# Kernel optimization log

Hardware: AMD Instinct MI355X
Metric: run time of the kernel (lower is better)

Reference implementation:

```python
import jax, jax.numpy as jnp
import numpy as np

B, S, H, E, K = 8, 4096, 1024, 256, 64
NEG = -1e30  # finite stand-in for -inf to keep grads NaN-free


def setup_inputs() -> dict:
    key = jax.random.key(0)
    ks = jax.random.split(key, 8)
    Hq = H // 4
    sc = 0.02
    return {
        "hidden_states": jax.random.normal(ks[0], (B, S, H), dtype=jnp.float32),
        "attention_mask": jnp.ones((B, S), dtype=jnp.int32),
        "block_boundaries": jnp.sort(jax.random.randint(ks[1], (B, K), 0, S), axis=-1),
        "tok_w1": jax.random.normal(ks[2], (H, Hq), dtype=jnp.float32) * sc,
        "tok_b1": jnp.zeros((Hq,), dtype=jnp.float32),
        "tok_w2": jax.random.normal(ks[3], (Hq, 1), dtype=jnp.float32) * sc,
        "tok_b2": jnp.zeros((1,), dtype=jnp.float32),
        "blk_w1": jax.random.normal(ks[4], (H, Hq), dtype=jnp.float32) * sc,
        "blk_b1": jnp.zeros((Hq,), dtype=jnp.float32),
        "blk_w2": jax.random.normal(ks[5], (Hq, 1), dtype=jnp.float32) * sc,
        "blk_b2": jnp.zeros((1,), dtype=jnp.float32),
        "out_w": jax.random.normal(ks[6], (H, E), dtype=jnp.float32) * sc,
        "out_b": jnp.zeros((E,), dtype=jnp.float32),
    }


def _attn_scores(x, w1, b1, w2, b2):
    # Linear -> Tanh -> Linear(.,1), squeeze last dim
    return (jnp.tanh(x @ w1 + b1) @ w2 + b2)[..., 0]


def reference(hidden_states, attention_mask, block_boundaries,
              tok_w1, tok_b1, tok_w2, tok_b2,
              blk_w1, blk_b1, blk_w2, blk_b2,
              out_w, out_b):
    Bz, Sz, Hz = hidden_states.shape
    Kz = block_boundaries.shape[1]
    pos = jnp.arange(Sz)
    # token -> block id: last boundary <= pos (tokens before first boundary get -1)
    block_id = jax.vmap(lambda bnd: jnp.searchsorted(bnd, pos, side='right') - 1)(block_boundaries)  # [B,S]
    member = block_id[:, :, None] == jnp.arange(Kz)[None, None, :]      # [B,S,K]
    valid = (attention_mask == 1) & (block_id >= 0)                     # [B,S]
    m_full = member & valid[:, :, None]                                 # [B,S,K]

    # stage 1: per-block masked softmax over tokens
    tok_scores = _attn_scores(hidden_states, tok_w1, tok_b1, tok_w2, tok_b2)  # [B,S]
    s = jnp.where(m_full, tok_scores[:, :, None], NEG)
    mx = jnp.max(s, axis=1, keepdims=True)                              # [B,1,K]
    e = jnp.where(m_full, jnp.exp(tok_scores[:, :, None] - mx), 0.0)
    denom = jnp.sum(e, axis=1, keepdims=True)                           # [B,1,K]
    w = jnp.where(denom > 0, e / jnp.maximum(denom, 1e-30), 0.0)
    block_embed = jnp.einsum('bsk,bsd->bkd', w, hidden_states)          # [B,K,H]
    block_valid = denom[:, 0, :] > 0                                    # [B,K] (empty blocks dropped)

    # stage 2: softmax over (non-empty) blocks
    blk_scores = _attn_scores(block_embed, blk_w1, blk_b1, blk_w2, blk_b2)    # [B,K]
    blk_scores = jnp.where(block_valid, blk_scores, NEG)
    bw = jax.nn.softmax(blk_scores, axis=-1)
    func = jnp.einsum('bk,bkd->bd', bw, block_embed)                    # [B,H]

    out = func @ out_w + out_b                                          # [B,E]
    return out / jnp.maximum(jnp.linalg.norm(out, axis=-1, keepdims=True), 1e-12)
```

## Files before the change

kernel.cpp:

```cpp
#include <hip/hip_runtime.h>
#include <math.h>

#define BB 8
#define SS 4096
#define HH 1024
#define EE 256
#define KK 64
#define HQ 256
#define NEGF -1e30f

typedef short bf16x8 __attribute__((ext_vector_type(8)));
typedef float f32x4  __attribute__((ext_vector_type(4)));

__device__ inline short f2bf(float x) {
    unsigned u = __float_as_uint(x);
    unsigned r = (u + 0x7fffu + ((u >> 16) & 1u)) >> 16;
    return (short)r;
}

__device__ inline unsigned pk2bf(float lo, float hi) {
    unsigned a = __float_as_uint(lo) + 0x8000u;
    unsigned b = __float_as_uint(hi) + 0x8000u;
    return (a >> 16) | (b & 0xffff0000u);
}

__global__ __launch_bounds__(256) void convert_w1_kernel(
    const float* __restrict__ w1, short* __restrict__ w1s)
{
    const int kb = blockIdx.x, n = threadIdx.x;
    for (int kk = 0; kk < 32; kk++)
        w1s[kb * 8192 + n * 32 + kk] = f2bf(w1[(kb * 32 + kk) * HQ + n]);
}

__global__ __launch_bounds__(256) void mfma_score3_kernel(
    const float* __restrict__ X, const short* __restrict__ w1s,
    const float* __restrict__ b1, const float* __restrict__ w2,
    const float* __restrict__ b2, float* __restrict__ out)
{
    __shared__ __attribute__((aligned(16))) short As[2][2048];
    __shared__ float part[4][64];

    const int t = threadIdx.x;
    const int wv = t >> 6, lane = t & 63, lo = lane & 15, q = lane >> 4;
    const long row0 = (long)blockIdx.x * 64;

    f32x4 acc[4][4];
#pragma unroll
    for (int i = 0; i < 4; i++)
#pragma unroll
        for (int j = 0; j < 4; j++) acc[i][j] = (f32x4){0.f, 0.f, 0.f, 0.f};

    const float* xs = X + (row0 + wv * 16 + lo) * HH + q * 8;
    const short* wp = w1s + (wv * 64 + lo) * 32 + q * 8;

    {
        const float4* p = (const float4*)xs;
        float4 v0 = p[0], v1 = p[1];
        union { unsigned u[4]; bf16x8 h; } c;
        c.u[0] = pk2bf(v0.x, v0.y); c.u[1] = pk2bf(v0.z, v0.w);
        c.u[2] = pk2bf(v1.x, v1.y); c.u[3] = pk2bf(v1.z, v1.w);
        *(bf16x8*)(&As[0][t * 8]) = c.h;
    }
    bf16x8 bA[4], bB[4];
#pragma unroll
    for (int ct = 0; ct < 4; ct++)
        bA[ct] = *(const bf16x8*)(wp + ct * 512);
    __syncthreads();

    for (int kb = 0; kb < 32; kb += 2) {
        {
            const int k1 = kb + 1;
            const float4* p = (const float4*)(xs + k1 * 32);
            float4 v0 = p[0], v1 = p[1];
#pragma unroll
            for (int ct = 0; ct < 4; ct++)
                bB[ct] = *(const bf16x8*)(wp + k1 * 8192 + ct * 512);
            bf16x8 af[4];
#pragma unroll
            for (int rt = 0; rt < 4; rt++)
                af[rt] = *(bf16x8*)(&As[0][(rt * 64 + q * 16 + lo) * 8]);
#pragma unroll
            for (int rt = 0; rt < 4; rt++)
#pragma unroll
                for (int ct = 0; ct < 4; ct++)
                    acc[rt][ct] = __builtin_amdgcn_mfma_f32_16x16x32_bf16(
                        af[rt], bA[ct], acc[rt][ct], 0, 0, 0);
            union { unsigned u[4]; bf16x8 h; } c;
            c.u[0] = pk2bf(v0.x, v0.y); c.u[1] = pk2bf(v0.z, v0.w);
            c.u[2] = pk2bf(v1.x, v1.y); c.u[3] = pk2bf(v1.z, v1.w);
            *(bf16x8*)(&As[1][t * 8]) = c.h;
        }
        __syncthreads();
        {
            const int k2 = (kb + 2 < 32) ? kb + 2 : 31;
            const float4* p = (const float4*)(xs + k2 * 32);
            float4 v0 = p[0], v1 = p[1];
#pragma unroll
            for (int ct = 0; ct < 4; ct++)
                bA[ct] = *(const bf16x8*)(wp + k2 * 8192 + ct * 512);
            bf16x8 af[4];
#pragma unroll
            for (int rt = 0; rt < 4; rt++)
                af[rt] = *(bf16x8*)(&As[1][(rt * 64 + q * 16 + lo) * 8]);
#pragma unroll
            for (int rt = 0; rt < 4; rt++)
#pragma unroll
                for (int ct = 0; ct < 4; ct++)
                    acc[rt][ct] = __builtin_amdgcn_mfma_f32_16x16x32_bf16(
                        af[rt], bB[ct], acc[rt][ct], 0, 0, 0);
            union { unsigned u[4]; bf16x8 h; } c;
            c.u[0] = pk2bf(v0.x, v0.y); c.u[1] = pk2bf(v0.z, v0.w);
            c.u[2] = pk2bf(v1.x, v1.y); c.u[3] = pk2bf(v1.z, v1.w);
            *(bf16x8*)(&As[0][t * 8]) = c.h;
        }
        __syncthreads();
    }

    float rowpart[4][4];
#pragma unroll
    for (int rt = 0; rt < 4; rt++)
#pragma unroll
        for (int r = 0; r < 4; r++) rowpart[rt][r] = 0.f;
#pragma unroll
    for (int ct = 0; ct < 4; ct++) {
        const int c = wv * 64 + ct * 16 + lo;
        const float b1c = b1[c], w2c = w2[c];
#pragma unroll
        for (int rt = 0; rt < 4; rt++)
#pragma unroll
            for (int r = 0; r < 4; r++)
                rowpart[rt][r] += tanhf(acc[rt][ct][r] + b1c) * w2c;
    }
#pragma unroll
    for (int rt = 0; rt < 4; rt++)
#pragma unroll
        for (int r = 0; r < 4; r++) {
            float v = rowpart[rt][r];
            v += __shfl_down(v, 8, 64);
            v += __shfl_down(v, 4, 64);
            v += __shfl_down(v, 2, 64);
            v += __shfl_down(v, 1, 64);
            rowpart[rt][r] = v;
        }
    if (lo == 0)
#pragma unroll
        for (int rt = 0; rt < 4; rt++)
#pragma unroll
            for (int r = 0; r < 4; r++)
                part[wv][rt * 16 + q * 4 + r] = rowpart[rt][r];
    __syncthreads();
    if (t < 64)
        out[row0 + t] = part[0][t] + part[1][t] + part[2][t] + part[3][t] + b2[0];
}

__global__ __launch_bounds__(256) void block_stats_kernel(
    const float* __restrict__ scores, const int* __restrict__ mask,
    const int* __restrict__ bnd, float* __restrict__ bmax, float* __restrict__ bden,
    float* __restrict__ wtok)
{
    const int b = blockIdx.x >> 6, k = blockIdx.x & 63;
    const int start = bnd[b * KK + k];
    const int end = (k == KK - 1) ? SS : bnd[b * KK + k + 1];
    const int tid = threadIdx.x;
    __shared__ float r[4];
    __shared__ float mshared, dshared;

    float m = NEGF;
    for (int s = start + tid; s < end; s += 256)
        if (mask[b * SS + s] == 1) m = fmaxf(m, scores[b * SS + s]);
    for (int off = 32; off > 0; off >>= 1) m = fmaxf(m, __shfl_down(m, off, 64));
    if ((tid & 63) == 0) r[tid >> 6] = m;
    __syncthreads();
    if (tid == 0) mshared = fmaxf(fmaxf(r[0], r[1]), fmaxf(r[2], r[3]));
    __syncthreads();
    m = mshared;

    float d = 0.f;
    for (int s = start + tid; s < end; s += 256)
        if (mask[b * SS + s] == 1) d += expf(scores[b * SS + s] - m);
    for (int off = 32; off > 0; off >>= 1) d += __shfl_down(d, off, 64);
    __syncthreads();
    if ((tid & 63) == 0) r[tid >> 6] = d;
    __syncthreads();
    if (tid == 0) {
        float den = r[0] + r[1] + r[2] + r[3];
        bmax[blockIdx.x] = m; bden[blockIdx.x] = den;
        dshared = (den > 0.f) ? 1.f / fmaxf(den, 1e-30f) : 0.f;
    }
    __syncthreads();
    const float inv = dshared;
    for (int s = start + tid; s < end; s += 256)
        wtok[b * SS + s] = (mask[b * SS + s] == 1) ? expf(scores[b * SS + s] - m) * inv : 0.f;
}

#define TCH 32
__global__ __launch_bounds__(256) void block_embed2_kernel(
    const float* __restrict__ hidden, const float* __restrict__ wtok,
    const int* __restrict__ bnd, float* __restrict__ embed)
{
    const int b = blockIdx.x >> 7;
    const int ch = blockIdx.x & 127;
    const int t = threadIdx.x;
    __shared__ int bsh[KK];
    if (t < KK) bsh[t] = bnd[b * KK + t];
    __syncthreads();

    const int s0 = ch * TCH, s1 = s0 + TCH;
    int cur = -1;
    for (int i = 0; i < KK; i++) if (bsh[i] <= s0) cur = i;

    float a0 = 0.f, a1 = 0.f, a2 = 0.f, a3 = 0.f;
    bool any = false;
    for (int s = s0; s < s1; s++) {
        while (cur + 1 < KK && bsh[cur + 1] <= s) {
            if (any) {
                float* e = embed + ((long)b * KK + cur) * HH;
                atomicAdd(e + t, a0); atomicAdd(e + t + 256, a1);
                atomicAdd(e + t + 512, a2); atomicAdd(e + t + 768, a3);
                a0 = a1 = a2 = a3 = 0.f; any = false;
            }
            cur++;
        }
        if (cur < 0) continue;
        const float w = wtok[b * SS + s];
        if (w != 0.f) {
            const float* hr = hidden + ((long)b * SS + s) * HH;
            a0 = fmaf(w, hr[t], a0);
            a1 = fmaf(w, hr[t + 256], a1);
            a2 = fmaf(w, hr[t + 512], a2);
            a3 = fmaf(w, hr[t + 768], a3);
            any = true;
        }
    }
    if (any) {
        float* e = embed + ((long)b * KK + cur) * HH;
        atomicAdd(e + t, a0); atomicAdd(e + t + 256, a1);
        atomicAdd(e + t + 512, a2); atomicAdd(e + t + 768, a3);
    }
}

__global__ __launch_bounds__(256) void finalize_a_kernel(
    const float* __restrict__ embed, const float* __restrict__ bscores,
    const float* __restrict__ bden, float* __restrict__ func)
{
    const int b = blockIdx.x, t = threadIdx.x;
    __shared__ float bw[KK];
    if (t < KK) {
        float s = (bden[b * KK + t] > 0.f) ? bscores[b * KK + t] : NEGF;
        float m = s;
        for (int off = 32; off > 0; off >>= 1) m = fmaxf(m, __shfl_xor(m, off, 64));
        float e = expf(s - m);
        float d = e;
        for (int off = 32; off > 0; off >>= 1) d += __shfl_xor(d, off, 64);
        bw[t] = e / d;
    }
    __syncthreads();
    float4 f = {0.f, 0.f, 0.f, 0.f};
    const float4* ep = (const float4*)(embed + (long)b * KK * HH) + t;
#pragma unroll 8
    for (int k = 0; k < KK; k++) {
        const float w = bw[k];
        const float4 h = ep[k * (HH / 4)];
        f.x = fmaf(w, h.x, f.x); f.y = fmaf(w, h.y, f.y);
        f.z = fmaf(w, h.z, f.z); f.w = fmaf(w, h.w, f.w);
    }
    *((float4*)(func + b * HH) + t) = f;
}

__global__ __launch_bounds__(256) void finalize_b_kernel(
    const float* __restrict__ func, const float* __restrict__ out_w,
    float* __restrict__ osum)
{
    const int b = blockIdx.x >> 3, hc = blockIdx.x & 7;
    const int t = threadIdx.x;
    __shared__ float fsh[128];
    if (t < 128) fsh[t] = func[b * HH + hc * 128 + t];
    __syncthreads();
    float acc = 0.f;
    const float* wp = out_w + (long)(hc * 128) * EE + t;
#pragma unroll 8
    for (int h = 0; h < 128; h++)
        acc = fmaf(fsh[h], wp[(long)h * EE], acc);
    atomicAdd(&osum[b * EE + t], acc);
}

__global__ __launch_bounds__(256) void finalize_c_kernel(
    const float* __restrict__ osum, const float* __restrict__ out_b,
    float* __restrict__ outp)
{
    const int b = blockIdx.x, t = threadIdx.x;
    __shared__ float r4[4];
    float o = osum[b * EE + t] + out_b[t];
    float sq = o * o;
    for (int off = 32; off > 0; off >>= 1) sq += __shfl_down(sq, off, 64);
    if ((t & 63) == 0) r4[t >> 6] = sq;
    __syncthreads();
    const float nrm = sqrtf(r4[0] + r4[1] + r4[2] + r4[3]);
    outp[b * EE + t] = o / fmaxf(nrm, 1e-12f);
}

extern "C" void kernel_launch(void* const* d_in, const int* in_sizes, int n_in,
                              void* d_out, int out_size, void* d_ws, size_t ws_size,
                              hipStream_t stream) {
    const float* hidden  = (const float*)d_in[0];
    const int*   mask    = (const int*)  d_in[1];
    const int*   bnd     = (const int*)  d_in[2];
    const float* tok_w1  = (const float*)d_in[3];
    const float* tok_b1  = (const float*)d_in[4];
    const float* tok_w2  = (const float*)d_in[5];
    const float* tok_b2  = (const float*)d_in[6];
    const float* blk_w1  = (const float*)d_in[7];
    const float* blk_b1  = (const float*)d_in[8];
    const float* blk_w2  = (const float*)d_in[9];
    const float* blk_b2  = (const float*)d_in[10];
    const float* out_w   = (const float*)d_in[11];
    const float* out_b   = (const float*)d_in[12];

    float* ws      = (float*)d_ws;
    float* wtok    = ws;
    float* embed   = ws + 32768;
    float* osum    = ws + 557056;
    float* scores  = ws + 559104;
    float* bmax    = ws + 591872;
    float* bden    = ws + 592384;
    float* bscores = ws + 592896;
    float* func    = ws + 593408;
    short* w1s     = (short*)(ws + 601600);

    hipMemsetAsync(d_ws, 0, (size_t)559104 * 4, stream);

    convert_w1_kernel<<<32, 256, 0, stream>>>(tok_w1, w1s);
    mfma_score3_kernel<<<BB * SS / 64, 256, 0, stream>>>(
        hidden, w1s, tok_b1, tok_w2, tok_b2, scores);
    block_stats_kernel<<<BB * KK, 256, 0, stream>>>(scores, mask, bnd, bmax, bden, wtok);
    block_embed2_kernel<<<BB * SS / TCH, 256, 0, stream>>>(hidden, wtok, bnd, embed);
    convert_w1_kernel<<<32, 256, 0, stream>>>(blk_w1, w1s);
    mfma_score3_kernel<<<BB * KK / 64, 256, 0, stream>>>(
        embed, w1s, blk_b1, blk_w2, blk_b2, bscores);
    finalize_a_kernel<<<BB, 256, 0, stream>>>(embed, bscores, bden, func);
    finalize_b_kernel<<<BB * 8, 256, 0, stream>>>(func, out_w, osum);
    finalize_c_kernel<<<BB, 256, 0, stream>>>(osum, out_b, (float*)d_out);
}
```

Before: 317.3 us.

## Shrink score tile, fuse weight conversions and finalizes, drop workspace memset

The score GEMM kernel now processes 32 rows per block instead of 64, with a new LDS staging layout and an occupancy hint of four blocks per SM, to double the grid. Both W1 conversions run in one launch. The workspace memset is removed: the embed and leading wtok zeroing move into block_stats, and finalize writes per-chunk partials instead of atomics. block_embed uses 16-token chunks with a fast path for chunks inside a single block and weights staged in shared memory. finalize_a and finalize_b are merged. The intent is fewer launches and better occupancy, at the cost of a smaller reuse tile in the GEMM and a redundant per-block weighted sum in the merged finalize.

```diff
diff --git a/kernel.cpp b/kernel.cpp
--- a/kernel.cpp
+++ b/kernel.cpp
@@ -1,5 +1,6 @@
 #include <hip/hip_runtime.h>
 #include <math.h>
+#include <limits.h>
 
 #define BB 8
 #define SS 4096
@@ -24,42 +25,48 @@
     return (a >> 16) | (b & 0xffff0000u);
 }
 
-__global__ __launch_bounds__(256) void convert_w1_kernel(
-    const float* __restrict__ w1, short* __restrict__ w1s)
-{
-    const int kb = blockIdx.x, n = threadIdx.x;
+__global__ __launch_bounds__(256) void convert_both_kernel(
+    const float* __restrict__ tok_w1, const float* __restrict__ blk_w1,
+    short* __restrict__ w1s_tok, short* __restrict__ w1s_blk)
+{
+    const int kb = blockIdx.x & 31, which = blockIdx.x >> 5;
+    const float* src = which ? blk_w1 : tok_w1;
+    short* dst = which ? w1s_blk : w1s_tok;
+    const int n = threadIdx.x;
     for (int kk = 0; kk < 32; kk++)
-        w1s[kb * 8192 + n * 32 + kk] = f2bf(w1[(kb * 32 + kk) * HQ + n]);
-}
-
-__global__ __launch_bounds__(256) void mfma_score3_kernel(
+        dst[kb * 8192 + n * 32 + kk] = f2bf(src[(kb * 32 + kk) * HQ + n]);
+}
+
+__global__ __launch_bounds__(256, 4) void mfma_score4_kernel(
     const float* __restrict__ X, const short* __restrict__ w1s,
     const float* __restrict__ b1, const float* __restrict__ w2,
     const float* __restrict__ b2, float* __restrict__ out)
 {
-    __shared__ __attribute__((aligned(16))) short As[2][2048];
-    __shared__ float part[4][64];
+    __shared__ __attribute__((aligned(16))) short As[2][1024];
+    __shared__ float part[4][32];
 
     const int t = threadIdx.x;
     const int wv = t >> 6, lane = t & 63, lo = lane & 15, q = lane >> 4;
-    const long row0 = (long)blockIdx.x * 64;
-
-    f32x4 acc[4][4];
-#pragma unroll
-    for (int i = 0; i < 4; i++)
+    const long row0 = (long)blockIdx.x * 32;
+
+    f32x4 acc[2][4];
+#pragma unroll
+    for (int i = 0; i < 2; i++)
 #pragma unroll
         for (int j = 0; j < 4; j++) acc[i][j] = (f32x4){0.f, 0.f, 0.f, 0.f};
 
-    const float* xs = X + (row0 + wv * 16 + lo) * HH + q * 8;
+    const int c = t >> 1, half = t & 1;
+    const int srow = ((c >> 6) << 4) + (c & 15);
+    const int skofs = ((c >> 4) & 3) * 8 + half * 4;
+    const float* xs = X + (row0 + srow) * HH + skofs;
+    short* const dst0 = &As[0][c * 8 + half * 4];
+    short* const dst1 = &As[1][c * 8 + half * 4];
     const short* wp = w1s + (wv * 64 + lo) * 32 + q * 8;
 
     {
-        const float4* p = (const float4*)xs;
-        float4 v0 = p[0], v1 = p[1];
-        union { unsigned u[4]; bf16x8 h; } c;
-        c.u[0] = pk2bf(v0.x, v0.y); c.u[1] = pk2bf(v0.z, v0.w);
-        c.u[2] = pk2bf(v1.x, v1.y); c.u[3] = pk2bf(v1.z, v1.w);
-        *(bf16x8*)(&As[0][t * 8]) = c.h;
+        float4 v = *(const float4*)xs;
+        unsigned u0 = pk2bf(v.x, v.y), u1 = pk2bf(v.z, v.w);
+        ((unsigned*)dst0)[0] = u0; ((unsigned*)dst0)[1] = u1;
     }
     bf16x8 bA[4], bB[4];
 #pragma unroll
@@ -69,70 +76,63 @@
 
     for (int kb = 0; kb < 32; kb += 2) {
         {
-            const int k1 = kb + 1;
-            const float4* p = (const float4*)(xs + k1 * 32);
-            float4 v0 = p[0], v1 = p[1];
+            float4 v = *(const float4*)(xs + (kb + 1) * 32);
 #pragma unroll
             for (int ct = 0; ct < 4; ct++)
-                bB[ct] = *(const bf16x8*)(wp + k1 * 8192 + ct * 512);
-            bf16x8 af[4];
-#pragma unroll
-            for (int rt = 0; rt < 4; rt++)
+                bB[ct] = *(const bf16x8*)(wp + (kb + 1) * 8192 + ct * 512);
+            bf16x8 af[2];
+#pragma unroll
+            for (int rt = 0; rt < 2; rt++)
                 af[rt] = *(bf16x8*)(&As[0][(rt * 64 + q * 16 + lo) * 8]);
 #pragma unroll
-            for (int rt = 0; rt < 4; rt++)
+            for (int rt = 0; rt < 2; rt++)
 #pragma unroll
                 for (int ct = 0; ct < 4; ct++)
                     acc[rt][ct] = __builtin_amdgcn_mfma_f32_16x16x32_bf16(
                         af[rt], bA[ct], acc[rt][ct], 0, 0, 0);
-            union { unsigned u[4]; bf16x8 h; } c;
-            c.u[0] = pk2bf(v0.x, v0.y); c.u[1] = pk2bf(v0.z, v0.w);
-            c.u[2] = pk2bf(v1.x, v1.y); c.u[3] = pk2bf(v1.z, v1.w);
-            *(bf16x8*)(&As[1][t * 8]) = c.h;
+            unsigned u0 = pk2bf(v.x, v.y), u1 = pk2bf(v.z, v.w);
+            ((unsigned*)dst1)[0] = u0; ((unsigned*)dst1)[1] = u1;
         }
         __syncthreads();
         {
             const int k2 = (kb + 2 < 32) ? kb + 2 : 31;
-            const float4* p = (const float4*)(xs + k2 * 32);
-            float4 v0 = p[0], v1 = p[1];
+            float4 v = *(const float4*)(xs + k2 * 32);
 #pragma unroll
             for (int ct = 0; ct < 4; ct++)
                 bA[ct] = *(const bf16x8*)(wp + k2 * 8192 + ct * 512);
-            bf16x8 af[4];
-#pragma unroll
-            for (int rt = 0; rt < 4; rt++)
+            bf16x8 af[2];
+#pragma unroll
+            for (int rt = 0; rt < 2; rt++)
                 af[rt] = *(bf16x8*)(&As[1][(rt * 64 + q * 16 + lo) * 8]);
 #pragma unroll
-            for (int rt = 0; rt < 4; rt++)
+            for (int rt = 0; rt < 2; rt++)
 #pragma unroll
                 for (int ct = 0; ct < 4; ct++)
                     acc[rt][ct] = __builtin_amdgcn_mfma_f32_16x16x32_bf16(
                         af[rt], bB[ct], acc[rt][ct], 0, 0, 0);
-            union { unsigned u[4]; bf16x8 h; } c;
-            c.u[0] = pk2bf(v0.x, v0.y); c.u[1] = pk2bf(v0.z, v0.w);
-            c.u[2] = pk2bf(v1.x, v1.y); c.u[3] = pk2bf(v1.z, v1.w);
-            *(bf16x8*)(&As[0][t * 8]) = c.h;
+            unsigned u0 = pk2bf(v.x, v.y), u1 = pk2bf(v.z, v.w);
+            ((unsigned*)dst0)[0] = u0; ((unsigned*)dst0)[1] = u1;
         }
         __syncthreads();
     }
 
-    float rowpart[4][4];
-#pragma unroll
-    for (int rt = 0; rt < 4; rt++)
+    float rowpart[2][4];
+#pragma unroll
+    for (int rt = 0; rt < 2; rt++)
 #pragma unroll
         for (int r = 0; r < 4; r++) rowpart[rt][r] = 0.f;
 #pragma unroll
     for (int ct = 0; ct < 4; ct++) {
-        const int c = wv * 64 + ct * 16 + lo;
-        const float b1c = b1[c], w2c = w2[c];
-#pragma unroll
-        for (int rt = 0; rt < 4; rt++)
+        const int cc = wv * 64 + ct * 16 + lo;
+        const float b1c = b1[cc], w2c = w2[cc];
+#pragma unroll
+        for (int rt = 0; rt < 2; rt++)
 #pragma unroll
             for (int r = 0; r < 4; r++)
                 rowpart[rt][r] += tanhf(acc[rt][ct][r] + b1c) * w2c;
     }
 #pragma unroll
-    for (int rt = 0; rt < 4; rt++)
+    for (int rt = 0; rt < 2; rt++)
 #pragma unroll
         for (int r = 0; r < 4; r++) {
             float v = rowpart[rt][r];
@@ -144,19 +144,19 @@
         }
     if (lo == 0)
 #pragma unroll
-        for (int rt = 0; rt < 4; rt++)
+        for (int rt = 0; rt < 2; rt++)
 #pragma unroll
             for (int r = 0; r < 4; r++)
                 part[wv][rt * 16 + q * 4 + r] = rowpart[rt][r];
     __syncthreads();
-    if (t < 64)
+    if (t < 32)
         out[row0 + t] = part[0][t] + part[1][t] + part[2][t] + part[3][t] + b2[0];
 }
 
 __global__ __launch_bounds__(256) void block_stats_kernel(
     const float* __restrict__ scores, const int* __restrict__ mask,
-    const int* __restrict__ bnd, float* __restrict__ bmax, float* __restrict__ bden,
-    float* __restrict__ wtok)
+    const int* __restrict__ bnd, float* __restrict__ bden,
+    float* __restrict__ wtok, float* __restrict__ embed)
 {
     const int b = blockIdx.x >> 6, k = blockIdx.x & 63;
     const int start = bnd[b * KK + k];
@@ -165,6 +165,10 @@
     __shared__ float r[4];
     __shared__ float mshared, dshared;
 
+    *((float4*)(embed + (long)blockIdx.x * HH) + tid) = (float4){0.f, 0.f, 0.f, 0.f};
+    if (k == 0)
+        for (int s = tid; s < start; s += 256) wtok[b * SS + s] = 0.f;
+
     float m = NEGF;
     for (int s = start + tid; s < end; s += 256)
         if (mask[b * SS + s] == 1) m = fmaxf(m, scores[b * SS + s]);
@@ -184,7 +188,7 @@
     __syncthreads();
     if (tid == 0) {
         float den = r[0] + r[1] + r[2] + r[3];
-        bmax[blockIdx.x] = m; bden[blockIdx.x] = den;
+        bden[blockIdx.x] = den;
         dshared = (den > 0.f) ? 1.f / fmaxf(den, 1e-30f) : 0.f;
     }
     __syncthreads();
@@ -193,23 +197,45 @@
         wtok[b * SS + s] = (mask[b * SS + s] == 1) ? expf(scores[b * SS + s] - m) * inv : 0.f;
 }
 
-#define TCH 32
-__global__ __launch_bounds__(256) void block_embed2_kernel(
+#define TCH 16
+__global__ __launch_bounds__(256) void block_embed4_kernel(
     const float* __restrict__ hidden, const float* __restrict__ wtok,
     const int* __restrict__ bnd, float* __restrict__ embed)
 {
-    const int b = blockIdx.x >> 7;
-    const int ch = blockIdx.x & 127;
+    const int b = blockIdx.x >> 8;
+    const int ch = blockIdx.x & 255;
     const int t = threadIdx.x;
     __shared__ int bsh[KK];
+    __shared__ float wsh[TCH];
+    const int s0 = ch * TCH, s1 = s0 + TCH;
     if (t < KK) bsh[t] = bnd[b * KK + t];
-    __syncthreads();
-
-    const int s0 = ch * TCH, s1 = s0 + TCH;
+    if (t >= 64 && t < 64 + TCH) wsh[t - 64] = wtok[b * SS + s0 + (t - 64)];
+    __syncthreads();
+
     int cur = -1;
-    for (int i = 0; i < KK; i++) if (bsh[i] <= s0) cur = i;
-
+#pragma unroll
+    for (int i = 0; i < KK; i++) cur = (bsh[i] <= s0) ? i : cur;
+    const int nxt = (cur + 1 < KK) ? bsh[cur + 1] : INT_MAX;
+
+    const float* hr0 = hidden + ((long)b * SS + s0) * HH + t;
     float a0 = 0.f, a1 = 0.f, a2 = 0.f, a3 = 0.f;
+
+    if (nxt >= s1 && cur >= 0) {
+#pragma unroll
+        for (int i = 0; i < TCH; i++) {
+            const float w = wsh[i];
+            const float* hr = hr0 + (long)i * HH;
+            a0 = fmaf(w, hr[0], a0);
+            a1 = fmaf(w, hr[256], a1);
+            a2 = fmaf(w, hr[512], a2);
+            a3 = fmaf(w, hr[768], a3);
+        }
+        float* e = embed + ((long)b * KK + cur) * HH;
+        atomicAdd(e + t, a0); atomicAdd(e + t + 256, a1);
+        atomicAdd(e + t + 512, a2); atomicAdd(e + t + 768, a3);
+        return;
+    }
+
     bool any = false;
     for (int s = s0; s < s1; s++) {
         while (cur + 1 < KK && bsh[cur + 1] <= s) {
@@ -222,15 +248,13 @@
             cur++;
         }
         if (cur < 0) continue;
-        const float w = wtok[b * SS + s];
-        if (w != 0.f) {
-            const float* hr = hidden + ((long)b * SS + s) * HH;
-            a0 = fmaf(w, hr[t], a0);
-            a1 = fmaf(w, hr[t + 256], a1);
-            a2 = fmaf(w, hr[t + 512], a2);
-            a3 = fmaf(w, hr[t + 768], a3);
-            any = true;
-        }
+        const float w = wsh[s - s0];
+        const float* hr = hr0 + (long)(s - s0) * HH;
+        a0 = fmaf(w, hr[0], a0);
+        a1 = fmaf(w, hr[256], a1);
+        a2 = fmaf(w, hr[512], a2);
+        a3 = fmaf(w, hr[768], a3);
+        any = true;
     }
     if (any) {
         float* e = embed + ((long)b * KK + cur) * HH;
@@ -239,12 +263,17 @@
     }
 }
 
-__global__ __launch_bounds__(256) void finalize_a_kernel(
+__global__ __launch_bounds__(256) void finalize_ab_kernel(
     const float* __restrict__ embed, const float* __restrict__ bscores,
-    const float* __restrict__ bden, float* __restrict__ func)
-{
-    const int b = blockIdx.x, t = threadIdx.x;
+    const float* __restrict__ bden, const float* __restrict__ out_w,
+    float* __restrict__ osum)
+{
+    const int b = blockIdx.x >> 3, hc = blockIdx.x & 7;
+    const int t = threadIdx.x;
     __shared__ float bw[KK];
+    __shared__ float fpart[2][128];
+    __shared__ float fsh[128];
+
     if (t < KK) {
         float s = (bden[b * KK + t] > 0.f) ? bscores[b * KK + t] : NEGF;
         float m = s;
@@ -255,33 +284,26 @@
         bw[t] = e / d;
     }
     __syncthreads();
-    float4 f = {0.f, 0.f, 0.f, 0.f};
-    const float4* ep = (const float4*)(embed + (long)b * KK * HH) + t;
+
+    {
+        const int hh = t & 127, kh = t >> 7;
+        const float* ep = embed + ((long)b * KK + kh * 32) * HH + hc * 128 + hh;
+        float f = 0.f;
 #pragma unroll 8
-    for (int k = 0; k < KK; k++) {
-        const float w = bw[k];
-        const float4 h = ep[k * (HH / 4)];
-        f.x = fmaf(w, h.x, f.x); f.y = fmaf(w, h.y, f.y);
-        f.z = fmaf(w, h.z, f.z); f.w = fmaf(w, h.w, f.w);
-    }
-    *((float4*)(func + b * HH) + t) = f;
-}
-
-__global__ __launch_bounds__(256) void finalize_b_kernel(
-    const float* __restrict__ func, const float* __restrict__ out_w,
-    float* __restrict__ osum)
-{
-    const int b = blockIdx.x >> 3, hc = blockIdx.x & 7;
-    const int t = threadIdx.x;
-    __shared__ float fsh[128];
-    if (t < 128) fsh[t] = func[b * HH + hc * 128 + t];
-    __syncthreads();
+        for (int k2 = 0; k2 < 32; k2++)
+            f = fmaf(bw[kh * 32 + k2], ep[(long)k2 * HH], f);
+        fpart[kh][hh] = f;
+    }
+    __syncthreads();
+    if (t < 128) fsh[t] = fpart[0][t] + fpart[1][t];
+    __syncthreads();
+
     float acc = 0.f;
-    const float* wp = out_w + (long)(hc * 128) * EE + t;
+    const float* wpp = out_w + (long)(hc * 128) * EE + t;
 #pragma unroll 8
     for (int h = 0; h < 128; h++)
-        acc = fmaf(fsh[h], wp[(long)h * EE], acc);
-    atomicAdd(&osum[b * EE + t], acc);
+        acc = fmaf(fsh[h], wpp[(long)h * EE], acc);
+    osum[(long)(b * 8 + hc) * EE + t] = acc;
 }
 
 __global__ __launch_bounds__(256) void finalize_c_kernel(
@@ -290,7 +312,10 @@
 {
     const int b = blockIdx.x, t = threadIdx.x;
     __shared__ float r4[4];
-    float o = osum[b * EE + t] + out_b[t];
+    float o = out_b[t];
+#pragma unroll
+    for (int hc = 0; hc < 8; hc++)
+        o += osum[(long)(b * 8 + hc) * EE + t];
     float sq = o * o;
     for (int off = 32; off > 0; off >>= 1) sq += __shfl_down(sq, off, 64);
     if ((t & 63) == 0) r4[t >> 6] = sq;
@@ -319,25 +344,22 @@
     float* ws      = (float*)d_ws;
     float* wtok    = ws;
     float* embed   = ws + 32768;
-    float* osum    = ws + 557056;
-    float* scores  = ws + 559104;
-    float* bmax    = ws + 591872;
-    float* bden    = ws + 592384;
-    float* bscores = ws + 592896;
-    float* func    = ws + 593408;
-    short* w1s     = (short*)(ws + 601600);
-
-    hipMemsetAsync(d_ws, 0, (size_t)559104 * 4, stream);
-
-    convert_w1_kernel<<<32, 256, 0, stream>>>(tok_w1, w1s);
-    mfma_score3_kernel<<<BB * SS / 64, 256, 0, stream>>>(
-        hidden, w1s, tok_b1, tok_w2, tok_b2, scores);
-    block_stats_kernel<<<BB * KK, 256, 0, stream>>>(scores, mask, bnd, bmax, bden, wtok);
-    block_embed2_kernel<<<BB * SS / TCH, 256, 0, stream>>>(hidden, wtok, bnd, embed);
-    convert_w1_kernel<<<32, 256, 0, stream>>>(blk_w1, w1s);
-    mfma_score3_kernel<<<BB * KK / 64, 256, 0, stream>>>(
-        embed, w1s, blk_b1, blk_w2, blk_b2, bscores);
-    finalize_a_kernel<<<BB, 256, 0, stream>>>(embed, bscores, bden, func);
-    finalize_b_kernel<<<BB * 8, 256, 0, stream>>>(func, out_w, osum);
+    float* scores  = ws + 557056;
+    float* bden    = ws + 589824;
+    float* bscores = ws + 590336;
+    float* osum    = ws + 590848;
+    short* w1s_tok = (short*)(ws + 607232);
+    short* w1s_blk = w1s_tok + 262144;
+
+    convert_both_kernel<<<64, 256, 0, stream>>>(tok_w1, blk_w1, w1s_tok, w1s_blk);
+    mfma_score4_kernel<<<BB * SS / 32, 256, 0, stream>>>(
+        hidden, w1s_tok, tok_b1, tok_w2, tok_b2, scores);
+    block_stats_kernel<<<BB * KK, 256, 0, stream>>>(
+        scores, mask, bnd, bden, wtok, embed);
+    block_embed4_kernel<<<BB * SS / TCH, 256, 0, stream>>>(hidden, wtok, bnd, embed);
+    mfma_score4_kernel<<<BB * KK / 32, 256, 0, stream>>>(
+        embed, w1s_blk, blk_b1, blk_w2, blk_b2, bscores);
+    finalize_ab_kernel<<<BB * 8, 256, 0, stream>>>(
+        embed, bscores, bden, out_w, osum);
     finalize_c_kernel<<<BB, 256, 0, stream>>>(osum, out_b, (float*)d_out);
 }
```

Measured after the change: 300.7 us. -5.2%, faster.
